# Kernel optimization log

Measured on AMD Instinct MI355X. Metric: run time of the kernel, lower is better.

Reference implementation:

```python
import jax, jax.numpy as jnp
import numpy as np

B, N, C, E, M = 16, 4096, 128, 12288, 64  # batch, nodes(seq_len), channels, incidences, hyperedges
NEG_SLOPE = 0.2
MARGIN = 4.2


def setup_inputs() -> dict:
    key = jax.random.key(0)
    k1, k2, k3, k4, k5 = jax.random.split(key, 5)
    x = jax.random.normal(k1, (B, N, C), jnp.float32)
    hyperedge_nodes = jax.random.randint(k2, (E,), 0, N)
    hyperedge_edges = jax.random.randint(k3, (E,), 0, M)
    weight = jax.random.normal(k4, (C, C), jnp.float32) * (1.0 / np.sqrt(C))  # glorot-ish
    att = jax.random.normal(k5, (1, 1, 2 * C), jnp.float32) * 0.1  # heads=1
    return {"x": x, "hyperedge_nodes": hyperedge_nodes, "hyperedge_edges": hyperedge_edges,
            "weight": weight, "att": att}


def _segment_softmax(logits, seg, num_segments):
    # logits: [E, B], softmax within groups of seg (per node)
    smax = jax.ops.segment_max(logits, seg, num_segments=num_segments)
    e = jnp.exp(logits - smax[seg])
    ssum = jax.ops.segment_sum(e, seg, num_segments=num_segments)
    return e / (ssum[seg] + 1e-16)


def reference(x, hyperedge_nodes, hyperedge_edges, weight, att):
    nodes = hyperedge_nodes
    edges = hyperedge_edges
    xw = jnp.matmul(x, weight)            # [B, N, C]
    x1 = jnp.swapaxes(xw, 0, 1)           # [N, B, C]

    x_gath = x1[nodes]                    # [E, B, C] gather by node id
    x_i = x_gath
    # per-hyperedge sum of incident node features (the python dict loop in torch)
    edge_sums = jax.ops.segment_sum(x_gath, edges, num_segments=M)  # [M, B, C]
    x_j = edge_sums[edges]                # [E, B, C]

    # O(M^2) pairwise hyperedge loss (vectorized)
    sq = jnp.sum(edge_sums * edge_sums, axis=-1)          # [M, B]
    norms = jnp.sqrt(sq)                                   # [M, B]
    inner = jnp.einsum('mbc,nbc->mnb', edge_sums, edge_sums)  # [M, M, B]
    cos = inner / (norms[:, None, :] * norms[None, :, :])      # [M, M, B]
    dist = jnp.sqrt(jnp.clip(sq[:, None, :] + sq[None, :, :] - 2.0 * inner, 0.0))
    loss_item = cos * dist + (1.0 - cos) * jnp.maximum(MARGIN - dist, 0.0)  # [M, M, B]
    loss_hyper = jnp.sum(jnp.abs(jnp.mean(loss_item, axis=-1))) / float((M + 1) ** 2)

    # attention per incidence, softmax grouped by node
    alpha = jnp.sum(jnp.concatenate([x_i, x_j], axis=-1) * att, axis=-1)  # [E, B]
    alpha = jax.nn.leaky_relu(alpha, NEG_SLOPE)
    alpha = _segment_softmax(alpha, nodes, N)  # [E, B] (dropout: eval mode, identity)

    ones = jnp.ones((E,), x.dtype)
    D = jax.ops.segment_sum(ones, nodes, num_segments=N)   # node degree
    Bdeg = jax.ops.segment_sum(ones, edges, num_segments=M)
    Bn = jnp.where(Bdeg > 0, 1.0 / Bdeg, 0.0)              # 1/deg, inf -> 0

    # propagate source_to_target: nodes -> hyperedges
    msg1 = Bn[edges][:, None, None] * x1[nodes] * alpha[:, :, None]   # [E, B, C]
    out_e = jax.ops.segment_sum(msg1, edges, num_segments=M)          # [M, B, C]
    # propagate target_to_source: hyperedges -> nodes
    msg2 = D[nodes][:, None, None] * out_e[edges] * alpha[:, :, None]
    out = jax.ops.segment_sum(msg2, nodes, num_segments=N)            # [N, B, C]
    out = jnp.swapaxes(out, 0, 1)                                     # [B, N, C]

    constrain_total = jnp.abs(jnp.mean(x_i - x_j)) + loss_hyper
    return (out, constrain_total)
```

## Files before the change

### kernel.cpp

```cpp
#include <hip/hip_runtime.h>
#include <hip/hip_bf16.h>

#define Bc 16
#define Nn 4096
#define Cc 128
#define Ee 12288
#define Mm 64
#define NEG_SLOPE 0.2f
#define MARGIN 4.2f
#define CH 4

typedef __attribute__((ext_vector_type(8))) short bfrag;
typedef __attribute__((ext_vector_type(4))) float f32x4;

__device__ inline unsigned short f2bf_rne(float f) {
    unsigned u = __float_as_uint(f);
    unsigned r = u + 0x7FFFu + ((u >> 16) & 1u);
    return (unsigned short)(r >> 16);
}
__device__ inline float bfbits2f(unsigned short h) {
    return __uint_as_float(((unsigned)h) << 16);
}

__global__ __launch_bounds__(256) void wsplit_kernel(const float* __restrict__ w,
                                                     unsigned short* __restrict__ wsplit) {
    int idx = blockIdx.x * 256 + threadIdx.x;
    int k = idx >> 7, c = idx & 127;
    float v = w[k * 128 + c];
    unsigned short h = f2bf_rne(v);
    float r = v - bfbits2f(h);
    unsigned short lo = f2bf_rne(r);
    int byteoff = c * 256 + ((2 * k) ^ ((c & 7) << 4));
    *(unsigned short*)((char*)wsplit + byteoff) = h;
    *(unsigned short*)((char*)wsplit + 32768 + byteoff) = lo;
}

__global__ __launch_bounds__(256) void gemm_xw(const float* __restrict__ x,
                                               const unsigned short* __restrict__ wsplit,
                                               const float* __restrict__ att,
                                               float* __restrict__ xw,
                                               float* __restrict__ p,
                                               float* __restrict__ S1) {
    __shared__ unsigned short wlds[32768];
    int t = threadIdx.x;
    {
        const float4* g4 = (const float4*)wsplit;
        float4* l4 = (float4*)wlds;
#pragma unroll
        for (int i = 0; i < 16; ++i) l4[i * 256 + t] = g4[i * 256 + t];
    }
    __syncthreads();

    int w = t >> 6;
    int l = t & 63;
    int lrow = l & 15;
    int lk = l >> 4;
    int rowbase = blockIdx.x * 128 + w * 32;

    f32x4 acc[2][8];
#pragma unroll
    for (int ti = 0; ti < 2; ++ti)
#pragma unroll
        for (int tj = 0; tj < 8; ++tj) acc[ti][tj] = (f32x4){0.f, 0.f, 0.f, 0.f};

    for (int ks = 0; ks < 4; ++ks) {
        bfrag bh[8], bl[8];
        int kbyte = (64 * ks + 16 * lk) ^ ((l & 7) << 4);
#pragma unroll
        for (int tj = 0; tj < 8; ++tj) {
            const char* base = (const char*)wlds + (tj * 16 + lrow) * 256 + kbyte;
            bh[tj] = *(const bfrag*)base;
            bl[tj] = *(const bfrag*)(base + 32768);
        }
#pragma unroll
        for (int ti = 0; ti < 2; ++ti) {
            int row = rowbase + ti * 16 + lrow;
            const float4* xp = (const float4*)(x + (size_t)row * 128 + ks * 32 + lk * 8);
            float4 v0 = xp[0], v1 = xp[1];
            float fa[8] = {v0.x, v0.y, v0.z, v0.w, v1.x, v1.y, v1.z, v1.w};
            bfrag ah, al;
#pragma unroll
            for (int j = 0; j < 8; ++j) {
                unsigned u = __float_as_uint(fa[j]);
                unsigned hb = u & 0xFFFF0000u;
                float r = fa[j] - __uint_as_float(hb);
                unsigned ru = __float_as_uint(r);
                unsigned r2 = ru + 0x7FFFu + ((ru >> 16) & 1u);
                ah[j] = (short)(hb >> 16);
                al[j] = (short)(r2 >> 16);
            }
#pragma unroll
            for (int tj = 0; tj < 8; ++tj) {
                acc[ti][tj] = __builtin_amdgcn_mfma_f32_16x16x32_bf16(ah, bh[tj], acc[ti][tj], 0, 0, 0);
                acc[ti][tj] = __builtin_amdgcn_mfma_f32_16x16x32_bf16(ah, bl[tj], acc[ti][tj], 0, 0, 0);
                acc[ti][tj] = __builtin_amdgcn_mfma_f32_16x16x32_bf16(al, bh[tj], acc[ti][tj], 0, 0, 0);
            }
        }
    }

    float aw_[8];
#pragma unroll
    for (int tj = 0; tj < 8; ++tj) aw_[tj] = att[tj * 16 + lrow];
#pragma unroll
    for (int ti = 0; ti < 2; ++ti) {
#pragma unroll
        for (int v = 0; v < 4; ++v) {
            int rr = rowbase + ti * 16 + lk * 4 + v;
            int b = rr >> 12;
            int n = rr & 4095;
            float* orow = xw + (size_t)n * 2048 + b * 128;
            float pd = 0.f, ss = 0.f;
#pragma unroll
            for (int tj = 0; tj < 8; ++tj) {
                float val = acc[ti][tj][v];
                orow[tj * 16 + lrow] = val;
                pd += val * aw_[tj];
                ss += val;
            }
#pragma unroll
            for (int m = 1; m < 16; m <<= 1) {
                pd += __shfl_xor(pd, m, 64);
                ss += __shfl_xor(ss, m, 64);
            }
            if (lrow == 0) {
                p[n * 16 + b] = pd;
                atomicAdd(&S1[n], ss);
            }
        }
    }
}

__global__ void hist_kernel(const int* __restrict__ nodes, const int* __restrict__ edges,
                            int* __restrict__ deg_n, int* __restrict__ deg_m) {
    int e = blockIdx.x * 256 + threadIdx.x;
    if (e < Ee) {
        atomicAdd(&deg_n[nodes[e]], 1);
        atomicAdd(&deg_m[edges[e]], 1);
    }
}

__global__ __launch_bounds__(1024) void scan_kernel(const int* __restrict__ deg_n,
                                                    const int* __restrict__ deg_m,
                                                    int* __restrict__ off_n, int* __restrict__ off_m,
                                                    int* __restrict__ cur_n, int* __restrict__ cur_m) {
    __shared__ int s[1024];
    int t = threadIdx.x;
    int base = t * 4;
    int d0 = deg_n[base], d1 = deg_n[base + 1], d2 = deg_n[base + 2], d3 = deg_n[base + 3];
    int local = d0 + d1 + d2 + d3;
    s[t] = local;
    __syncthreads();
    for (int offs = 1; offs < 1024; offs <<= 1) {
        int v = (t >= offs) ? s[t - offs] : 0;
        __syncthreads();
        s[t] += v;
        __syncthreads();
    }
    int excl = s[t] - local;
    int o0 = excl, o1 = excl + d0, o2 = excl + d0 + d1, o3 = excl + d0 + d1 + d2;
    off_n[base] = o0; off_n[base + 1] = o1; off_n[base + 2] = o2; off_n[base + 3] = o3;
    cur_n[base] = o0; cur_n[base + 1] = o1; cur_n[base + 2] = o2; cur_n[base + 3] = o3;
    if (t == 1023) off_n[4096] = s[1023];
    if (t == 0) {
        int acc = 0;
        for (int m = 0; m < 64; m++) {
            off_m[m] = acc; cur_m[m] = acc; acc += deg_m[m];
        }
        off_m[64] = acc;
    }
}

__global__ void fill_kernel(const int* __restrict__ nodes, const int* __restrict__ edges,
                            int* __restrict__ cur_n, int* __restrict__ cur_m,
                            int* __restrict__ list_n, int* __restrict__ gedge_n,
                            int* __restrict__ list_m, int* __restrict__ gnode_m) {
    int e = blockIdx.x * 256 + threadIdx.x;
    if (e < Ee) {
        int n = nodes[e], m = edges[e];
        int pos = atomicAdd(&cur_n[n], 1);
        list_n[pos] = e;
        gedge_n[pos] = m;
        int pos2 = atomicAdd(&cur_m[m], 1);
        list_m[pos2] = e;
        gnode_m[pos2] = n;
    }
}

__global__ __launch_bounds__(256) void edge_sums_kernel(const float* __restrict__ xw,
                                                        const int* __restrict__ off_m,
                                                        const int* __restrict__ gnode_m,
                                                        float* __restrict__ es) {
    int m = blockIdx.x;
    int slot = blockIdx.y * 256 + threadIdx.x;
    int beg = off_m[m], end = off_m[m + 1];
    int len = end - beg;
    int cbeg = beg + (len * (int)blockIdx.z) / CH;
    int cend = beg + (len * ((int)blockIdx.z + 1)) / CH;
    float acc = 0.f;
    for (int i = cbeg; i < cend; i++) {
        int n = gnode_m[i];
        acc += xw[(size_t)n * 2048 + slot];
    }
    if (acc != 0.f || cend > cbeg) atomicAdd(&es[m * 2048 + slot], acc);
}

__global__ __launch_bounds__(256) void edge_stats_kernel(const float* __restrict__ es,
                                                         const float* __restrict__ att,
                                                         float* __restrict__ q,
                                                         float* __restrict__ sq,
                                                         float* __restrict__ T) {
    int m = blockIdx.x, t = threadIdx.x;
    int b = t >> 4, oc = (t & 15) * 8;
    const float* row = es + m * 2048 + b * 128 + oc;
    float qd = 0.f, sqd = 0.f, s = 0.f;
#pragma unroll
    for (int j = 0; j < 8; j++) {
        float v = row[j];
        qd += v * att[128 + oc + j];
        sqd += v * v;
        s += v;
    }
    for (int k = 1; k < 16; k <<= 1) {
        qd += __shfl_xor(qd, k, 64);
        sqd += __shfl_xor(sqd, k, 64);
        s += __shfl_xor(s, k, 64);
    }
    if ((t & 15) == 0) { q[m * 16 + b] = qd; sq[m * 16 + b] = sqd; }
    s += __shfl_xor(s, 16, 64);
    s += __shfl_xor(s, 32, 64);
    __shared__ float ws4[4];
    if ((t & 63) == 0) ws4[t >> 6] = s;
    __syncthreads();
    if (t == 0) T[m] = ws4[0] + ws4[1] + ws4[2] + ws4[3];
}

__global__ __launch_bounds__(256) void loss_kernel(const float* __restrict__ es,
                                                   const float* __restrict__ sq,
                                                   float* __restrict__ loss_part) {
    int m = blockIdx.x, t = threadIdx.x;
    __shared__ float esm[2048];
    for (int i = t; i < 2048; i += 256) esm[i] = es[m * 2048 + i];
    __syncthreads();
    int n = t >> 2, bq = t & 3;
    float part = 0.f;
#pragma unroll
    for (int u = 0; u < 4; u++) {
        int b = bq * 4 + u;
        float inner = 0.f;
        const float* er = es + n * 2048 + b * 128;
        const float* em = esm + b * 128;
        for (int c = 0; c < 128; c += 4) {
            float4 a = *(const float4*)(em + c);
            float4 o = *(const float4*)(er + c);
            inner += a.x * o.x + a.y * o.y + a.z * o.z + a.w * o.w;
        }
        float sm = sq[m * 16 + b], sn = sq[n * 16 + b];
        float cosv = inner / (sqrtf(sm) * sqrtf(sn));
        float d2 = sm + sn - 2.f * inner;
        float dist = sqrtf(fmaxf(d2, 0.f));
        part += cosv * dist + (1.f - cosv) * fmaxf(MARGIN - dist, 0.f);
    }
    part += __shfl_xor(part, 1, 64);
    part += __shfl_xor(part, 2, 64);
    float labs = fabsf(part * (1.f / 16.f));
    __shared__ float pl[64];
    if (bq == 0) pl[n] = labs;
    __syncthreads();
    if (t < 64) {
        float v = pl[t];
        for (int k = 1; k < 64; k <<= 1) v += __shfl_xor(v, k, 64);
        if (t == 0) loss_part[m] = v;
    }
}

__global__ __launch_bounds__(256) void alpha_kernel(const int* __restrict__ off_n,
                                                    const int* __restrict__ list_n,
                                                    const int* __restrict__ gedge_n,
                                                    const float* __restrict__ p,
                                                    const float* __restrict__ q,
                                                    float* __restrict__ alpha) {
    int idx = blockIdx.x * 256 + threadIdx.x;
    int b = idx & 15, n = idx >> 4;
    int beg = off_n[n], end = off_n[n + 1];
    if (beg == end) return;
    float pb = p[n * 16 + b];
    float lf = pb + q[gedge_n[beg] * 16 + b];
    lf = lf >= 0.f ? lf : NEG_SLOPE * lf;
    float ssum = 0.f;
    for (int i = beg; i < end; i++) {
        float l = pb + q[gedge_n[i] * 16 + b];
        l = l >= 0.f ? l : NEG_SLOPE * l;
        ssum += __expf(l - lf);
    }
    float inv = 1.f / ssum;
    for (int i = beg; i < end; i++) {
        int e = list_n[i];
        float l = pb + q[gedge_n[i] * 16 + b];
        l = l >= 0.f ? l : NEG_SLOPE * l;
        alpha[e * 16 + b] = __expf(l - lf) * inv;
    }
}

__global__ __launch_bounds__(256) void out_e_kernel(const float* __restrict__ xw,
                                                    const int* __restrict__ off_m,
                                                    const int* __restrict__ list_m,
                                                    const int* __restrict__ gnode_m,
                                                    const float* __restrict__ alpha,
                                                    float* __restrict__ oute) {
    int m = blockIdx.x;
    int slot = blockIdx.y * 256 + threadIdx.x;
    int b = slot >> 7;
    int beg = off_m[m], end = off_m[m + 1];
    int len = end - beg;
    int cbeg = beg + (len * (int)blockIdx.z) / CH;
    int cend = beg + (len * ((int)blockIdx.z + 1)) / CH;
    float acc = 0.f;
    for (int i = cbeg; i < cend; i++) {
        int n = gnode_m[i];
        int e = list_m[i];
        acc += alpha[e * 16 + b] * xw[(size_t)n * 2048 + slot];
    }
    if (cend > cbeg) atomicAdd(&oute[m * 2048 + slot], acc);
}

__global__ __launch_bounds__(256) void out_kernel(const float* __restrict__ oute,
                                                  const int* __restrict__ off_n,
                                                  const int* __restrict__ list_n,
                                                  const int* __restrict__ gedge_n,
                                                  const int* __restrict__ deg_m,
                                                  const float* __restrict__ alpha,
                                                  float* __restrict__ out) {
    int n = blockIdx.x, t = threadIdx.x;
    int beg = off_n[n], end = off_n[n + 1];
    float d = (float)(end - beg);
    float acc[8] = {0, 0, 0, 0, 0, 0, 0, 0};
    for (int i = beg; i < end; i++) {
        int e = list_n[i];
        int m = gedge_n[i];
        float bn = 1.f / (float)deg_m[m];
        const float* er = oute + m * 2048;
#pragma unroll
        for (int k = 0; k < 8; k++) {
            int slot = t + k * 256;
            int b = slot >> 7;
            acc[k] += alpha[e * 16 + b] * bn * er[slot];
        }
    }
#pragma unroll
    for (int k = 0; k < 8; k++) {
        int slot = t + k * 256;
        int b = slot >> 7, c = slot & 127;
        out[(size_t)b * 524288 + n * 128 + c] = d * acc[k];
    }
}

__global__ __launch_bounds__(256) void finalize_kernel(const int* __restrict__ deg_n,
                                                       const float* __restrict__ S1,
                                                       const int* __restrict__ deg_m,
                                                       const float* __restrict__ T,
                                                       const float* __restrict__ loss_part,
                                                       float* __restrict__ out_scalar) {
    int t = threadIdx.x;
    double a = 0.0;
    for (int n = t; n < 4096; n += 256) a += (double)deg_n[n] * (double)S1[n];
    double bsum = 0.0, l = 0.0;
    if (t < 64) {
        bsum = (double)deg_m[t] * (double)T[t];
        l = (double)loss_part[t];
    }
    __shared__ double sa[256], sb[256], sl[256];
    sa[t] = a; sb[t] = bsum; sl[t] = l;
    __syncthreads();
    for (int s = 128; s > 0; s >>= 1) {
        if (t < s) { sa[t] += sa[t + s]; sb[t] += sb[t + s]; sl[t] += sl[t + s]; }
        __syncthreads();
    }
    if (t == 0) {
        double mean = (sa[0] - sb[0]) / 25165824.0;
        out_scalar[0] = (float)(fabs(mean) + sl[0] / 4225.0);
    }
}

extern "C" void kernel_launch(void* const* d_in, const int* in_sizes, int n_in,
                              void* d_out, int out_size, void* d_ws, size_t ws_size,
                              hipStream_t stream) {
    const float* x = (const float*)d_in[0];
    const int* nodes = (const int*)d_in[1];
    const int* edges = (const int*)d_in[2];
    const float* w = (const float*)d_in[3];
    const float* att = (const float*)d_in[4];
    float* out = (float*)d_out;

    char* ws = (char*)d_ws;
    size_t o = 0;
    float* xw = (float*)(ws + o);        o += (size_t)Nn * Bc * Cc * 4;
    size_t zbase = o;
    float* es = (float*)(ws + o);        o += (size_t)Mm * Bc * Cc * 4;
    float* oute = (float*)(ws + o);      o += (size_t)Mm * Bc * Cc * 4;
    int* deg_n = (int*)(ws + o);         o += (size_t)Nn * 4;
    int* deg_m = (int*)(ws + o);         o += (size_t)Mm * 4;
    float* S1 = (float*)(ws + o);        o += (size_t)Nn * 4;
    size_t zlen = o - zbase;
    float* p = (float*)(ws + o);         o += (size_t)Nn * Bc * 4;
    float* q = (float*)(ws + o);         o += (size_t)Mm * Bc * 4;
    float* sq = (float*)(ws + o);        o += (size_t)Mm * Bc * 4;
    float* alpha = (float*)(ws + o);     o += (size_t)Ee * Bc * 4;
    unsigned short* wsplit = (unsigned short*)(ws + o); o += 65536;
    float* T = (float*)(ws + o);         o += (size_t)Mm * 4;
    float* loss_part = (float*)(ws + o); o += (size_t)Mm * 4;
    int* off_n = (int*)(ws + o);         o += (size_t)(Nn + 1) * 4;
    int* off_m = (int*)(ws + o);         o += (size_t)(Mm + 1) * 4;
    int* cur_n = (int*)(ws + o);         o += (size_t)Nn * 4;
    int* cur_m = (int*)(ws + o);         o += (size_t)Mm * 4;
    int* list_n = (int*)(ws + o);        o += (size_t)Ee * 4;
    int* gedge_n = (int*)(ws + o);       o += (size_t)Ee * 4;
    int* list_m = (int*)(ws + o);        o += (size_t)Ee * 4;
    int* gnode_m = (int*)(ws + o);       o += (size_t)Ee * 4;

    hipMemsetAsync(ws + zbase, 0, zlen, stream);

    wsplit_kernel<<<64, 256, 0, stream>>>(w, wsplit);
    gemm_xw<<<512, 256, 0, stream>>>(x, wsplit, att, xw, p, S1);
    hist_kernel<<<48, 256, 0, stream>>>(nodes, edges, deg_n, deg_m);
    scan_kernel<<<1, 1024, 0, stream>>>(deg_n, deg_m, off_n, off_m, cur_n, cur_m);
    fill_kernel<<<48, 256, 0, stream>>>(nodes, edges, cur_n, cur_m,
                                        list_n, gedge_n, list_m, gnode_m);
    edge_sums_kernel<<<dim3(Mm, 8, CH), 256, 0, stream>>>(xw, off_m, gnode_m, es);
    edge_stats_kernel<<<Mm, 256, 0, stream>>>(es, att, q, sq, T);
    loss_kernel<<<Mm, 256, 0, stream>>>(es, sq, loss_part);
    alpha_kernel<<<256, 256, 0, stream>>>(off_n, list_n, gedge_n, p, q, alpha);
    out_e_kernel<<<dim3(Mm, 8, CH), 256, 0, stream>>>(xw, off_m, list_m, gnode_m, alpha, oute);
    out_kernel<<<Nn, 256, 0, stream>>>(oute, off_n, list_n, gedge_n, deg_m, alpha, out);
    finalize_kernel<<<1, 256, 0, stream>>>(deg_n, S1, deg_m, T, loss_part, out + (size_t)Bc * Nn * Cc);
}
```

Measured before the change: 243.4 us.

## Replace gather/scatter segment sums with dense incidence-matrix MFMA GEMMs

Builds a dense node-hyperedge count matrix and dense attention-weight matrices, then computes edge sums, hyperedge outputs and node outputs as split-bf16 MFMA GEMMs over a transposed bf16 hi/lo copy of xW. It also merges the weight split with the degree histogram and drops the per-hyperedge CSR lists and the sq buffer, which loss_kernel now recomputes itself. The aim is to swap irregular gathers and atomics for tensor-core matmuls. In exchange it zeroes and streams large dense Wa/Wb buffers of mostly zeros and runs es_gemm with few blocks.

```diff
diff --git a/kernel.cpp b/kernel.cpp
--- a/kernel.cpp
+++ b/kernel.cpp
@@ -8,7 +8,6 @@
 #define Mm 64
 #define NEG_SLOPE 0.2f
 #define MARGIN 4.2f
-#define CH 4
 
 typedef __attribute__((ext_vector_type(8))) short bfrag;
 typedef __attribute__((ext_vector_type(4))) float f32x4;
@@ -21,24 +20,55 @@
 __device__ inline float bfbits2f(unsigned short h) {
     return __uint_as_float(((unsigned)h) << 16);
 }
-
-__global__ __launch_bounds__(256) void wsplit_kernel(const float* __restrict__ w,
-                                                     unsigned short* __restrict__ wsplit) {
-    int idx = blockIdx.x * 256 + threadIdx.x;
-    int k = idx >> 7, c = idx & 127;
-    float v = w[k * 128 + c];
-    unsigned short h = f2bf_rne(v);
-    float r = v - bfbits2f(h);
-    unsigned short lo = f2bf_rne(r);
-    int byteoff = c * 256 + ((2 * k) ^ ((c & 7) << 4));
-    *(unsigned short*)((char*)wsplit + byteoff) = h;
-    *(unsigned short*)((char*)wsplit + 32768 + byteoff) = lo;
+__device__ inline void split1(float f, unsigned short& h, unsigned short& lo) {
+    unsigned u = __float_as_uint(f);
+    unsigned hb = u & 0xFFFF0000u;
+    float r = f - __uint_as_float(hb);
+    unsigned ru = __float_as_uint(r);
+    ru += 0x7FFFu + ((ru >> 16) & 1u);
+    h = (unsigned short)(u >> 16);
+    lo = (unsigned short)(ru >> 16);
+}
+__device__ inline void split8(const float* f, bfrag& h, bfrag& l) {
+#pragma unroll
+    for (int j = 0; j < 8; ++j) {
+        unsigned short hh, ll;
+        split1(f[j], hh, ll);
+        h[j] = (short)hh; l[j] = (short)ll;
+    }
+}
+
+__global__ __launch_bounds__(256) void prep_kernel(const float* __restrict__ w,
+                                                   const int* __restrict__ nodes,
+                                                   const int* __restrict__ edges,
+                                                   unsigned short* __restrict__ wsplit,
+                                                   int* __restrict__ deg_n,
+                                                   int* __restrict__ deg_m,
+                                                   float* __restrict__ Acnt) {
+    int blk = blockIdx.x, t = threadIdx.x;
+    if (blk < 64) {
+        int idx = blk * 256 + t;
+        int k = idx >> 7, c = idx & 127;
+        float v = w[k * 128 + c];
+        unsigned short h, lo;
+        split1(v, h, lo);
+        int byteoff = c * 256 + ((2 * k) ^ ((c & 7) << 4));
+        *(unsigned short*)((char*)wsplit + byteoff) = h;
+        *(unsigned short*)((char*)wsplit + 32768 + byteoff) = lo;
+    } else {
+        int e = (blk - 64) * 256 + t;
+        int n = nodes[e], m = edges[e];
+        atomicAdd(&deg_n[n], 1);
+        atomicAdd(&deg_m[m], 1);
+        atomicAdd(&Acnt[m * 4096 + n], 1.0f);
+    }
 }
 
 __global__ __launch_bounds__(256) void gemm_xw(const float* __restrict__ x,
                                                const unsigned short* __restrict__ wsplit,
                                                const float* __restrict__ att,
-                                               float* __restrict__ xw,
+                                               unsigned short* __restrict__ xwTh,
+                                               unsigned short* __restrict__ xwTl,
                                                float* __restrict__ p,
                                                float* __restrict__ S1) {
     __shared__ unsigned short wlds[32768];
@@ -51,10 +81,8 @@
     }
     __syncthreads();
 
-    int w = t >> 6;
-    int l = t & 63;
-    int lrow = l & 15;
-    int lk = l >> 4;
+    int w = t >> 6, l = t & 63;
+    int lrow = l & 15, lk = l >> 4;
     int rowbase = blockIdx.x * 128 + w * 32;
 
     f32x4 acc[2][8];
@@ -81,13 +109,9 @@
             bfrag ah, al;
 #pragma unroll
             for (int j = 0; j < 8; ++j) {
-                unsigned u = __float_as_uint(fa[j]);
-                unsigned hb = u & 0xFFFF0000u;
-                float r = fa[j] - __uint_as_float(hb);
-                unsigned ru = __float_as_uint(r);
-                unsigned r2 = ru + 0x7FFFu + ((ru >> 16) & 1u);
-                ah[j] = (short)(hb >> 16);
-                al[j] = (short)(r2 >> 16);
+                unsigned short hh, ll;
+                split1(fa[j], hh, ll);
+                ah[j] = (short)hh; al[j] = (short)ll;
             }
 #pragma unroll
             for (int tj = 0; tj < 8; ++tj) {
@@ -98,6 +122,22 @@
         }
     }
 
+#pragma unroll
+    for (int ti = 0; ti < 2; ++ti) {
+#pragma unroll
+        for (int tj = 0; tj < 8; ++tj) {
+            int rr0 = rowbase + ti * 16 + lk * 4;
+            int b = rr0 >> 12, n0 = rr0 & 4095;
+            int slot = b * 128 + tj * 16 + lrow;
+            ushort4 hv, lv;
+            split1(acc[ti][tj][0], hv.x, lv.x);
+            split1(acc[ti][tj][1], hv.y, lv.y);
+            split1(acc[ti][tj][2], hv.z, lv.z);
+            split1(acc[ti][tj][3], hv.w, lv.w);
+            *(ushort4*)(xwTh + (size_t)slot * 4096 + n0) = hv;
+            *(ushort4*)(xwTl + (size_t)slot * 4096 + n0) = lv;
+        }
+    }
     float aw_[8];
 #pragma unroll
     for (int tj = 0; tj < 8; ++tj) aw_[tj] = att[tj * 16 + lrow];
@@ -106,14 +146,11 @@
 #pragma unroll
         for (int v = 0; v < 4; ++v) {
             int rr = rowbase + ti * 16 + lk * 4 + v;
-            int b = rr >> 12;
-            int n = rr & 4095;
-            float* orow = xw + (size_t)n * 2048 + b * 128;
+            int b = rr >> 12, n = rr & 4095;
             float pd = 0.f, ss = 0.f;
 #pragma unroll
             for (int tj = 0; tj < 8; ++tj) {
                 float val = acc[ti][tj][v];
-                orow[tj * 16 + lrow] = val;
                 pd += val * aw_[tj];
                 ss += val;
             }
@@ -130,19 +167,9 @@
     }
 }
 
-__global__ void hist_kernel(const int* __restrict__ nodes, const int* __restrict__ edges,
-                            int* __restrict__ deg_n, int* __restrict__ deg_m) {
-    int e = blockIdx.x * 256 + threadIdx.x;
-    if (e < Ee) {
-        atomicAdd(&deg_n[nodes[e]], 1);
-        atomicAdd(&deg_m[edges[e]], 1);
-    }
-}
-
 __global__ __launch_bounds__(1024) void scan_kernel(const int* __restrict__ deg_n,
-                                                    const int* __restrict__ deg_m,
-                                                    int* __restrict__ off_n, int* __restrict__ off_m,
-                                                    int* __restrict__ cur_n, int* __restrict__ cur_m) {
+                                                    int* __restrict__ off_n,
+                                                    int* __restrict__ cur_n) {
     __shared__ int s[1024];
     int t = threadIdx.x;
     int base = t * 4;
@@ -161,100 +188,109 @@
     off_n[base] = o0; off_n[base + 1] = o1; off_n[base + 2] = o2; off_n[base + 3] = o3;
     cur_n[base] = o0; cur_n[base + 1] = o1; cur_n[base + 2] = o2; cur_n[base + 3] = o3;
     if (t == 1023) off_n[4096] = s[1023];
-    if (t == 0) {
-        int acc = 0;
-        for (int m = 0; m < 64; m++) {
-            off_m[m] = acc; cur_m[m] = acc; acc += deg_m[m];
-        }
-        off_m[64] = acc;
-    }
 }
 
 __global__ void fill_kernel(const int* __restrict__ nodes, const int* __restrict__ edges,
-                            int* __restrict__ cur_n, int* __restrict__ cur_m,
-                            int* __restrict__ list_n, int* __restrict__ gedge_n,
-                            int* __restrict__ list_m, int* __restrict__ gnode_m) {
+                            int* __restrict__ cur_n, int* __restrict__ gedge_n) {
     int e = blockIdx.x * 256 + threadIdx.x;
     if (e < Ee) {
-        int n = nodes[e], m = edges[e];
-        int pos = atomicAdd(&cur_n[n], 1);
-        list_n[pos] = e;
-        gedge_n[pos] = m;
-        int pos2 = atomicAdd(&cur_m[m], 1);
-        list_m[pos2] = e;
-        gnode_m[pos2] = n;
-    }
-}
-
-__global__ __launch_bounds__(256) void edge_sums_kernel(const float* __restrict__ xw,
-                                                        const int* __restrict__ off_m,
-                                                        const int* __restrict__ gnode_m,
-                                                        float* __restrict__ es) {
-    int m = blockIdx.x;
-    int slot = blockIdx.y * 256 + threadIdx.x;
-    int beg = off_m[m], end = off_m[m + 1];
-    int len = end - beg;
-    int cbeg = beg + (len * (int)blockIdx.z) / CH;
-    int cend = beg + (len * ((int)blockIdx.z + 1)) / CH;
-    float acc = 0.f;
-    for (int i = cbeg; i < cend; i++) {
-        int n = gnode_m[i];
-        acc += xw[(size_t)n * 2048 + slot];
-    }
-    if (acc != 0.f || cend > cbeg) atomicAdd(&es[m * 2048 + slot], acc);
-}
-
-__global__ __launch_bounds__(256) void edge_stats_kernel(const float* __restrict__ es,
-                                                         const float* __restrict__ att,
-                                                         float* __restrict__ q,
-                                                         float* __restrict__ sq,
-                                                         float* __restrict__ T) {
-    int m = blockIdx.x, t = threadIdx.x;
-    int b = t >> 4, oc = (t & 15) * 8;
-    const float* row = es + m * 2048 + b * 128 + oc;
-    float qd = 0.f, sqd = 0.f, s = 0.f;
-#pragma unroll
-    for (int j = 0; j < 8; j++) {
-        float v = row[j];
-        qd += v * att[128 + oc + j];
-        sqd += v * v;
-        s += v;
-    }
-    for (int k = 1; k < 16; k <<= 1) {
-        qd += __shfl_xor(qd, k, 64);
-        sqd += __shfl_xor(sqd, k, 64);
-        s += __shfl_xor(s, k, 64);
-    }
-    if ((t & 15) == 0) { q[m * 16 + b] = qd; sq[m * 16 + b] = sqd; }
-    s += __shfl_xor(s, 16, 64);
-    s += __shfl_xor(s, 32, 64);
-    __shared__ float ws4[4];
-    if ((t & 63) == 0) ws4[t >> 6] = s;
-    __syncthreads();
-    if (t == 0) T[m] = ws4[0] + ws4[1] + ws4[2] + ws4[3];
+        int pos = atomicAdd(&cur_n[nodes[e]], 1);
+        gedge_n[pos] = edges[e];
+    }
+}
+
+__global__ __launch_bounds__(256) void es_gemm(const float* __restrict__ Acnt,
+                                               const unsigned short* __restrict__ xwTh,
+                                               const unsigned short* __restrict__ xwTl,
+                                               const float* __restrict__ att,
+                                               float* __restrict__ es,
+                                               float* __restrict__ q,
+                                               float* __restrict__ T) {
+    int t = threadIdx.x, w = t >> 6, l = t & 63;
+    int lrow = l & 15, lk = l >> 4;
+    int slot0 = blockIdx.x * 64;
+    f32x4 acc[4];
+#pragma unroll
+    for (int tj = 0; tj < 4; ++tj) acc[tj] = (f32x4){0.f, 0.f, 0.f, 0.f};
+    const float* arow = Acnt + (size_t)(w * 16 + lrow) * 4096;
+#pragma unroll 2
+    for (int ks = 0; ks < 128; ++ks) {
+        int n0 = ks * 32 + lk * 8;
+        const float* ap = arow + n0;
+        bfrag af;
+#pragma unroll
+        for (int j = 0; j < 8; ++j) af[j] = (short)(__float_as_uint(ap[j]) >> 16);
+#pragma unroll
+        for (int tj = 0; tj < 4; ++tj) {
+            size_t off = (size_t)(slot0 + tj * 16 + lrow) * 4096 + n0;
+            bfrag bh = *(const bfrag*)(xwTh + off);
+            bfrag bl = *(const bfrag*)(xwTl + off);
+            acc[tj] = __builtin_amdgcn_mfma_f32_16x16x32_bf16(af, bh, acc[tj], 0, 0, 0);
+            acc[tj] = __builtin_amdgcn_mfma_f32_16x16x32_bf16(af, bl, acc[tj], 0, 0, 0);
+        }
+    }
+    int b = slot0 >> 7;
+    float qp[4] = {0, 0, 0, 0}, tp[4] = {0, 0, 0, 0};
+#pragma unroll
+    for (int tj = 0; tj < 4; ++tj) {
+        int slot = slot0 + tj * 16 + lrow;
+        float a2 = att[128 + (slot & 127)];
+#pragma unroll
+        for (int reg = 0; reg < 4; ++reg) {
+            int mm = w * 16 + lk * 4 + reg;
+            float val = acc[tj][reg];
+            es[mm * 2048 + slot] = val;
+            qp[reg] += val * a2;
+            tp[reg] += val;
+        }
+    }
+#pragma unroll
+    for (int msk = 1; msk < 16; msk <<= 1) {
+#pragma unroll
+        for (int reg = 0; reg < 4; ++reg) {
+            qp[reg] += __shfl_xor(qp[reg], msk, 64);
+            tp[reg] += __shfl_xor(tp[reg], msk, 64);
+        }
+    }
+    if (lrow == 0) {
+#pragma unroll
+        for (int reg = 0; reg < 4; ++reg) {
+            int mm = w * 16 + lk * 4 + reg;
+            atomicAdd(&q[mm * 16 + b], qp[reg]);
+            atomicAdd(&T[mm], tp[reg]);
+        }
+    }
 }
 
 __global__ __launch_bounds__(256) void loss_kernel(const float* __restrict__ es,
-                                                   const float* __restrict__ sq,
                                                    float* __restrict__ loss_part) {
     int m = blockIdx.x, t = threadIdx.x;
     __shared__ float esm[2048];
+    __shared__ float sml[16];
     for (int i = t; i < 2048; i += 256) esm[i] = es[m * 2048 + i];
+    __syncthreads();
+    if (t < 16) {
+        float s = 0.f;
+        const float* r = esm + t * 128;
+        for (int c = 0; c < 128; ++c) s += r[c] * r[c];
+        sml[t] = s;
+    }
     __syncthreads();
     int n = t >> 2, bq = t & 3;
     float part = 0.f;
 #pragma unroll
     for (int u = 0; u < 4; u++) {
         int b = bq * 4 + u;
-        float inner = 0.f;
+        float inner = 0.f, sn = 0.f;
         const float* er = es + n * 2048 + b * 128;
         const float* em = esm + b * 128;
         for (int c = 0; c < 128; c += 4) {
             float4 a = *(const float4*)(em + c);
             float4 o = *(const float4*)(er + c);
             inner += a.x * o.x + a.y * o.y + a.z * o.z + a.w * o.w;
-        }
-        float sm = sq[m * 16 + b], sn = sq[n * 16 + b];
+            sn += o.x * o.x + o.y * o.y + o.z * o.z + o.w * o.w;
+        }
+        float sm = sml[b];
         float cosv = inner / (sqrtf(sm) * sqrtf(sn));
         float d2 = sm + sn - 2.f * inner;
         float dist = sqrtf(fmaxf(d2, 0.f));
@@ -273,12 +309,13 @@
     }
 }
 
-__global__ __launch_bounds__(256) void alpha_kernel(const int* __restrict__ off_n,
-                                                    const int* __restrict__ list_n,
-                                                    const int* __restrict__ gedge_n,
-                                                    const float* __restrict__ p,
-                                                    const float* __restrict__ q,
-                                                    float* __restrict__ alpha) {
+__global__ __launch_bounds__(256) void alpha_wab(const int* __restrict__ off_n,
+                                                 const int* __restrict__ gedge_n,
+                                                 const float* __restrict__ p,
+                                                 const float* __restrict__ q,
+                                                 const int* __restrict__ deg_m,
+                                                 float* __restrict__ Wa,
+                                                 float* __restrict__ Wb) {
     int idx = blockIdx.x * 256 + threadIdx.x;
     int b = idx & 15, n = idx >> 4;
     int beg = off_n[n], end = off_n[n + 1];
@@ -288,69 +325,110 @@
     lf = lf >= 0.f ? lf : NEG_SLOPE * lf;
     float ssum = 0.f;
     for (int i = beg; i < end; i++) {
-        float l = pb + q[gedge_n[i] * 16 + b];
-        l = l >= 0.f ? l : NEG_SLOPE * l;
-        ssum += __expf(l - lf);
+        float lg = pb + q[gedge_n[i] * 16 + b];
+        lg = lg >= 0.f ? lg : NEG_SLOPE * lg;
+        ssum += __expf(lg - lf);
     }
     float inv = 1.f / ssum;
     for (int i = beg; i < end; i++) {
-        int e = list_n[i];
-        float l = pb + q[gedge_n[i] * 16 + b];
-        l = l >= 0.f ? l : NEG_SLOPE * l;
-        alpha[e * 16 + b] = __expf(l - lf) * inv;
-    }
-}
-
-__global__ __launch_bounds__(256) void out_e_kernel(const float* __restrict__ xw,
-                                                    const int* __restrict__ off_m,
-                                                    const int* __restrict__ list_m,
-                                                    const int* __restrict__ gnode_m,
-                                                    const float* __restrict__ alpha,
-                                                    float* __restrict__ oute) {
-    int m = blockIdx.x;
-    int slot = blockIdx.y * 256 + threadIdx.x;
-    int b = slot >> 7;
-    int beg = off_m[m], end = off_m[m + 1];
-    int len = end - beg;
-    int cbeg = beg + (len * (int)blockIdx.z) / CH;
-    int cend = beg + (len * ((int)blockIdx.z + 1)) / CH;
-    float acc = 0.f;
-    for (int i = cbeg; i < cend; i++) {
-        int n = gnode_m[i];
-        int e = list_m[i];
-        acc += alpha[e * 16 + b] * xw[(size_t)n * 2048 + slot];
-    }
-    if (cend > cbeg) atomicAdd(&oute[m * 2048 + slot], acc);
-}
-
-__global__ __launch_bounds__(256) void out_kernel(const float* __restrict__ oute,
-                                                  const int* __restrict__ off_n,
-                                                  const int* __restrict__ list_n,
-                                                  const int* __restrict__ gedge_n,
-                                                  const int* __restrict__ deg_m,
-                                                  const float* __restrict__ alpha,
-                                                  float* __restrict__ out) {
-    int n = blockIdx.x, t = threadIdx.x;
-    int beg = off_n[n], end = off_n[n + 1];
-    float d = (float)(end - beg);
-    float acc[8] = {0, 0, 0, 0, 0, 0, 0, 0};
-    for (int i = beg; i < end; i++) {
-        int e = list_n[i];
         int m = gedge_n[i];
-        float bn = 1.f / (float)deg_m[m];
-        const float* er = oute + m * 2048;
-#pragma unroll
-        for (int k = 0; k < 8; k++) {
-            int slot = t + k * 256;
-            int b = slot >> 7;
-            acc[k] += alpha[e * 16 + b] * bn * er[slot];
-        }
-    }
-#pragma unroll
-    for (int k = 0; k < 8; k++) {
-        int slot = t + k * 256;
-        int b = slot >> 7, c = slot & 127;
-        out[(size_t)b * 524288 + n * 128 + c] = d * acc[k];
+        float lg = pb + q[m * 16 + b];
+        lg = lg >= 0.f ? lg : NEG_SLOPE * lg;
+        float a = __expf(lg - lf) * inv;
+        float bninv = 1.f / (float)deg_m[m];
+        atomicAdd(&Wa[((size_t)b * 64 + m) * 4096 + n], a);
+        atomicAdd(&Wb[((size_t)b * 4096 + n) * 64 + m], a * bninv);
+    }
+}
+
+__global__ __launch_bounds__(256) void oute_gemm(const unsigned short* __restrict__ xwTh,
+                                                 const unsigned short* __restrict__ xwTl,
+                                                 const float* __restrict__ Wa,
+                                                 float* __restrict__ ouT) {
+    int t = threadIdx.x, w = t >> 6, l = t & 63;
+    int lrow = l & 15, lk = l >> 4;
+    int slot0 = blockIdx.x * 64;
+    int b = slot0 >> 7;
+    int kbase = blockIdx.y * 1024;
+    f32x4 acc[4];
+#pragma unroll
+    for (int tj = 0; tj < 4; ++tj) acc[tj] = (f32x4){0.f, 0.f, 0.f, 0.f};
+    int srow = slot0 + w * 16 + lrow;
+    const unsigned short* xh = xwTh + (size_t)srow * 4096;
+    const unsigned short* xl = xwTl + (size_t)srow * 4096;
+    const float* wab = Wa + (size_t)b * 64 * 4096;
+#pragma unroll 2
+    for (int ks = 0; ks < 32; ++ks) {
+        int n0 = kbase + ks * 32 + lk * 8;
+        bfrag ah = *(const bfrag*)(xh + n0);
+        bfrag al = *(const bfrag*)(xl + n0);
+#pragma unroll
+        for (int tj = 0; tj < 4; ++tj) {
+            int mcol = tj * 16 + lrow;
+            bfrag wh, wl_;
+            split8(wab + (size_t)mcol * 4096 + n0, wh, wl_);
+            acc[tj] = __builtin_amdgcn_mfma_f32_16x16x32_bf16(ah, wh, acc[tj], 0, 0, 0);
+            acc[tj] = __builtin_amdgcn_mfma_f32_16x16x32_bf16(ah, wl_, acc[tj], 0, 0, 0);
+            acc[tj] = __builtin_amdgcn_mfma_f32_16x16x32_bf16(al, wh, acc[tj], 0, 0, 0);
+        }
+    }
+#pragma unroll
+    for (int tj = 0; tj < 4; ++tj) {
+        int mcol = tj * 16 + lrow;
+#pragma unroll
+        for (int reg = 0; reg < 4; ++reg) {
+            int slot = slot0 + w * 16 + lk * 4 + reg;
+            atomicAdd(&ouT[slot * 64 + mcol], acc[tj][reg]);
+        }
+    }
+}
+
+__global__ __launch_bounds__(256) void out_gemm(const float* __restrict__ Wb,
+                                                const float* __restrict__ ouT,
+                                                const int* __restrict__ deg_n,
+                                                float* __restrict__ out) {
+    int t = threadIdx.x, w = t >> 6, l = t & 63;
+    int lrow = l & 15, lk = l >> 4;
+    int nbase = blockIdx.x * 128 + w * 32;
+    int b = blockIdx.y;
+    f32x4 acc[2][8];
+#pragma unroll
+    for (int ti = 0; ti < 2; ++ti)
+#pragma unroll
+        for (int tj = 0; tj < 8; ++tj) acc[ti][tj] = (f32x4){0.f, 0.f, 0.f, 0.f};
+#pragma unroll
+    for (int ks = 0; ks < 2; ++ks) {
+        int m0 = ks * 32 + lk * 8;
+        bfrag wh[2], wl[2];
+#pragma unroll
+        for (int ti = 0; ti < 2; ++ti) {
+            int nr = nbase + ti * 16 + lrow;
+            split8(Wb + ((size_t)b * 4096 + nr) * 64 + m0, wh[ti], wl[ti]);
+        }
+#pragma unroll
+        for (int tj = 0; tj < 8; ++tj) {
+            int slot = b * 128 + tj * 16 + lrow;
+            bfrag oh, ol;
+            split8(ouT + (size_t)slot * 64 + m0, oh, ol);
+#pragma unroll
+            for (int ti = 0; ti < 2; ++ti) {
+                acc[ti][tj] = __builtin_amdgcn_mfma_f32_16x16x32_bf16(wh[ti], oh, acc[ti][tj], 0, 0, 0);
+                acc[ti][tj] = __builtin_amdgcn_mfma_f32_16x16x32_bf16(wh[ti], ol, acc[ti][tj], 0, 0, 0);
+                acc[ti][tj] = __builtin_amdgcn_mfma_f32_16x16x32_bf16(wl[ti], oh, acc[ti][tj], 0, 0, 0);
+            }
+        }
+    }
+#pragma unroll
+    for (int ti = 0; ti < 2; ++ti) {
+#pragma unroll
+        for (int reg = 0; reg < 4; ++reg) {
+            int n = nbase + ti * 16 + lk * 4 + reg;
+            float d = (float)deg_n[n];
+#pragma unroll
+            for (int tj = 0; tj < 8; ++tj) {
+                out[(size_t)b * 524288 + (size_t)n * 128 + tj * 16 + lrow] = d * acc[ti][tj][reg];
+            }
+        }
     }
 }
 
@@ -363,13 +441,13 @@
     int t = threadIdx.x;
     double a = 0.0;
     for (int n = t; n < 4096; n += 256) a += (double)deg_n[n] * (double)S1[n];
-    double bsum = 0.0, l = 0.0;
+    double bsum = 0.0, lsum = 0.0;
     if (t < 64) {
         bsum = (double)deg_m[t] * (double)T[t];
-        l = (double)loss_part[t];
+        lsum = (double)loss_part[t];
     }
     __shared__ double sa[256], sb[256], sl[256];
-    sa[t] = a; sb[t] = bsum; sl[t] = l;
+    sa[t] = a; sb[t] = bsum; sl[t] = lsum;
     __syncthreads();
     for (int s = 128; s > 0; s >>= 1) {
         if (t < s) { sa[t] += sa[t + s]; sb[t] += sb[t + s]; sl[t] += sl[t + s]; }
@@ -393,43 +471,37 @@
 
     char* ws = (char*)d_ws;
     size_t o = 0;
-    float* xw = (float*)(ws + o);        o += (size_t)Nn * Bc * Cc * 4;
+    unsigned short* xwTh = (unsigned short*)(ws + o); o += (size_t)2048 * 4096 * 2;
+    unsigned short* xwTl = (unsigned short*)(ws + o); o += (size_t)2048 * 4096 * 2;
     size_t zbase = o;
-    float* es = (float*)(ws + o);        o += (size_t)Mm * Bc * Cc * 4;
-    float* oute = (float*)(ws + o);      o += (size_t)Mm * Bc * Cc * 4;
-    int* deg_n = (int*)(ws + o);         o += (size_t)Nn * 4;
-    int* deg_m = (int*)(ws + o);         o += (size_t)Mm * 4;
-    float* S1 = (float*)(ws + o);        o += (size_t)Nn * 4;
+    float* Acnt = (float*)(ws + o);  o += (size_t)Mm * Nn * 4;
+    float* Wa = (float*)(ws + o);    o += (size_t)Bc * Mm * Nn * 4;
+    float* Wb = (float*)(ws + o);    o += (size_t)Bc * Nn * Mm * 4;
+    float* ouT = (float*)(ws + o);   o += (size_t)2048 * 64 * 4;
+    int* deg_n = (int*)(ws + o);     o += (size_t)Nn * 4;
+    int* deg_m = (int*)(ws + o);     o += (size_t)Mm * 4;
+    float* S1 = (float*)(ws + o);    o += (size_t)Nn * 4;
+    float* q = (float*)(ws + o);     o += (size_t)Mm * Bc * 4;
+    float* T = (float*)(ws + o);     o += (size_t)Mm * 4;
     size_t zlen = o - zbase;
+    float* es = (float*)(ws + o);        o += (size_t)Mm * 2048 * 4;
     float* p = (float*)(ws + o);         o += (size_t)Nn * Bc * 4;
-    float* q = (float*)(ws + o);         o += (size_t)Mm * Bc * 4;
-    float* sq = (float*)(ws + o);        o += (size_t)Mm * Bc * 4;
-    float* alpha = (float*)(ws + o);     o += (size_t)Ee * Bc * 4;
-    unsigned short* wsplit = (unsigned short*)(ws + o); o += 65536;
-    float* T = (float*)(ws + o);         o += (size_t)Mm * 4;
     float* loss_part = (float*)(ws + o); o += (size_t)Mm * 4;
     int* off_n = (int*)(ws + o);         o += (size_t)(Nn + 1) * 4;
-    int* off_m = (int*)(ws + o);         o += (size_t)(Mm + 1) * 4;
     int* cur_n = (int*)(ws + o);         o += (size_t)Nn * 4;
-    int* cur_m = (int*)(ws + o);         o += (size_t)Mm * 4;
-    int* list_n = (int*)(ws + o);        o += (size_t)Ee * 4;
     int* gedge_n = (int*)(ws + o);       o += (size_t)Ee * 4;
-    int* list_m = (int*)(ws + o);        o += (size_t)Ee * 4;
-    int* gnode_m = (int*)(ws + o);       o += (size_t)Ee * 4;
+    unsigned short* wsplit = (unsigned short*)(ws + o); o += 65536;
 
     hipMemsetAsync(ws + zbase, 0, zlen, stream);
 
-    wsplit_kernel<<<64, 256, 0, stream>>>(w, wsplit);
-    gemm_xw<<<512, 256, 0, stream>>>(x, wsplit, att, xw, p, S1);
-    hist_kernel<<<48, 256, 0, stream>>>(nodes, edges, deg_n, deg_m);
-    scan_kernel<<<1, 1024, 0, stream>>>(deg_n, deg_m, off_n, off_m, cur_n, cur_m);
-    fill_kernel<<<48, 256, 0, stream>>>(nodes, edges, cur_n, cur_m,
-                                        list_n, gedge_n, list_m, gnode_m);
-    edge_sums_kernel<<<dim3(Mm, 8, CH), 256, 0, stream>>>(xw, off_m, gnode_m, es);
-    edge_stats_kernel<<<Mm, 256, 0, stream>>>(es, att, q, sq, T);
-    loss_kernel<<<Mm, 256, 0, stream>>>(es, sq, loss_part);
-    alpha_kernel<<<256, 256, 0, stream>>>(off_n, list_n, gedge_n, p, q, alpha);
-    out_e_kernel<<<dim3(Mm, 8, CH), 256, 0, stream>>>(xw, off_m, list_m, gnode_m, alpha, oute);
-    out_kernel<<<Nn, 256, 0, stream>>>(oute, off_n, list_n, gedge_n, deg_m, alpha, out);
+    prep_kernel<<<112, 256, 0, stream>>>(w, nodes, edges, wsplit, deg_n, deg_m, Acnt);
+    gemm_xw<<<512, 256, 0, stream>>>(x, wsplit, att, xwTh, xwTl, p, S1);
+    scan_kernel<<<1, 1024, 0, stream>>>(deg_n, off_n, cur_n);
+    fill_kernel<<<48, 256, 0, stream>>>(nodes, edges, cur_n, gedge_n);
+    es_gemm<<<32, 256, 0, stream>>>(Acnt, xwTh, xwTl, att, es, q, T);
+    loss_kernel<<<Mm, 256, 0, stream>>>(es, loss_part);
+    alpha_wab<<<256, 256, 0, stream>>>(off_n, gedge_n, p, q, deg_m, Wa, Wb);
+    oute_gemm<<<dim3(32, 4), 256, 0, stream>>>(xwTh, xwTl, Wa, ouT);
+    out_gemm<<<dim3(32, 16), 256, 0, stream>>>(Wb, ouT, deg_n, out);
     finalize_kernel<<<1, 256, 0, stream>>>(deg_n, S1, deg_m, T, loss_part, out + (size_t)Bc * Nn * Cc);
 }
```

Result: slower. 392.3 us (+61.2%).
